# Performance work log

Measured on AMD Instinct MI355X. Metric: run time of the kernel, lower is better.

The kernel has to match this reference:

```python
import jax, jax.numpy as jnp
import numpy as np

B, N, C, H = 16, 800, 1024, 16
NC = 128  # cached KV length from the N==128 pass
HD = C // H


def setup_inputs() -> dict:
    key = jax.random.key(0)
    ks = jax.random.split(key, 9)
    s = 0.02  # init scale for weights
    return {
        "x": jax.random.normal(ks[0], (B, N, C), jnp.float32),
        "xpos": jax.random.normal(ks[1], (B, N, C), jnp.float32),
        "k_t": jax.random.normal(ks[2], (B, NC, C), jnp.float32),
        "v_t": jax.random.normal(ks[3], (B, NC, C), jnp.float32),
        "Wq": jax.random.normal(ks[4], (C, C), jnp.float32) * s,
        "Wk": jax.random.normal(ks[5], (C, C), jnp.float32) * s,
        "Wv": jax.random.normal(ks[6], (C, C), jnp.float32) * s,
        "Wp": jax.random.normal(ks[7], (C, C), jnp.float32) * s,
        "bp": jnp.zeros((C,), jnp.float32),
    }


def reference(x, xpos, k_t, v_t, Wq, Wk, Wv, Wp, bp):
    # N == 800 branch: q from x+xpos; k/v concat cached k_t/v_t before projection.
    b, n, c = x.shape
    scale = HD ** -0.5

    q = (x + xpos) @ Wq.T                              # [B, N, C]
    k_in = jnp.concatenate([x + xpos, k_t], axis=1)    # [B, N+NC, C]
    v_in = jnp.concatenate([x, v_t], axis=1)           # [B, N+NC, C]
    k = k_in @ Wk.T
    v = v_in @ Wv.T

    def heads(t):
        return t.reshape(b, t.shape[1], H, HD).transpose(0, 2, 1, 3)  # [B,H,L,HD]

    qh, kh, vh = heads(q), heads(k), heads(v)
    attn = jax.nn.softmax(jnp.einsum('bhqd,bhkd->bhqk', qh, kh) * scale, axis=-1)
    out = jnp.einsum('bhqk,bhkd->bhqd', attn, vh)       # [B,H,N,HD]
    out = out.transpose(0, 2, 1, 3).reshape(b, n, c)
    return out @ Wp.T + bp
```

## Files before the change

kernel.cpp:

```cpp
#include <hip/hip_runtime.h>
#include <hip/hip_bf16.h>

#define NB 16
#define NN 800
#define NCACHE 128
#define NL 928
#define CC 1024
#define NH 16
#define HD 64

typedef __attribute__((ext_vector_type(8))) short bf16x8;
typedef __attribute__((ext_vector_type(4))) float f32x4;
typedef __attribute__((ext_vector_type(2))) __bf16 bf2;

__device__ __forceinline__ short f2bf(float x) {
  union { float f; unsigned u; } c; c.f = x;
  unsigned r = c.u + 0x7fffu + ((c.u >> 16) & 1u);
  return (short)(r >> 16);
}

#define GLD_LDS(gp, lp) __builtin_amdgcn_global_load_lds( \
    (__attribute__((address_space(1))) void*)(gp),        \
    (__attribute__((address_space(3))) void*)(lp), 16, 0, 0)

#define BAR() asm volatile("s_barrier" ::: "memory")

__global__ __launch_bounds__(256) void prep_kv(
    const float* __restrict__ x, const float* __restrict__ xpos,
    const float* __restrict__ ktc, const float* __restrict__ vtc,
    short* __restrict__ k_in, short* __restrict__ v_in) {
  int idx = blockIdx.x * 256 + threadIdx.x;
  int chunk = idx & 127;
  int row = idx >> 7;
  int b = row / NL;
  int lr = row - b * NL;
  int c = chunk * 8;
  float vk[8], vv[8];
  if (lr < NN) {
    const float4* px = (const float4*)(x + ((size_t)(b * NN + lr) * CC + c));
    const float4* pp = (const float4*)(xpos + ((size_t)(b * NN + lr) * CC + c));
    float4 x0 = px[0], x1 = px[1], p0 = pp[0], p1 = pp[1];
    vv[0]=x0.x; vv[1]=x0.y; vv[2]=x0.z; vv[3]=x0.w;
    vv[4]=x1.x; vv[5]=x1.y; vv[6]=x1.z; vv[7]=x1.w;
    vk[0]=x0.x+p0.x; vk[1]=x0.y+p0.y; vk[2]=x0.z+p0.z; vk[3]=x0.w+p0.w;
    vk[4]=x1.x+p1.x; vk[5]=x1.y+p1.y; vk[6]=x1.z+p1.z; vk[7]=x1.w+p1.w;
  } else {
    const float4* pk = (const float4*)(ktc + ((size_t)(b * NCACHE + lr - NN) * CC + c));
    const float4* pv = (const float4*)(vtc + ((size_t)(b * NCACHE + lr - NN) * CC + c));
    float4 k0 = pk[0], k1 = pk[1], v0 = pv[0], v1 = pv[1];
    vk[0]=k0.x; vk[1]=k0.y; vk[2]=k0.z; vk[3]=k0.w;
    vk[4]=k1.x; vk[5]=k1.y; vk[6]=k1.z; vk[7]=k1.w;
    vv[0]=v0.x; vv[1]=v0.y; vv[2]=v0.z; vv[3]=v0.w;
    vv[4]=v1.x; vv[5]=v1.y; vv[6]=v1.z; vv[7]=v1.w;
  }
  bf16x8 ok, ov;
#pragma unroll
  for (int i = 0; i < 8; ++i) { ok[i] = f2bf(vk[i]); ov[i] = f2bf(vv[i]); }
  *(bf16x8*)(k_in + (size_t)row * CC + c) = ok;
  *(bf16x8*)(v_in + (size_t)row * CC + c) = ov;
}

__global__ __launch_bounds__(256) void prep_w(
    const float* __restrict__ Wq, const float* __restrict__ Wk,
    const float* __restrict__ Wv, const float* __restrict__ Wp,
    short* __restrict__ wout) {
  int idx = blockIdx.x * 256 + threadIdx.x;
  int wsel = idx >> 17;
  int off = (idx & 131071) * 8;
  const float* src = wsel == 0 ? Wq : wsel == 1 ? Wk : wsel == 2 ? Wv : Wp;
  float sc = wsel == 0 ? 0.18033688011112042f : 1.0f;
  const float4* p = (const float4*)(src + off);
  float4 a = p[0], b = p[1];
  bf16x8 o;
  o[0]=f2bf(a.x*sc); o[1]=f2bf(a.y*sc); o[2]=f2bf(a.z*sc); o[3]=f2bf(a.w*sc);
  o[4]=f2bf(b.x*sc); o[5]=f2bf(b.y*sc); o[6]=f2bf(b.z*sc); o[7]=f2bf(b.w*sc);
  *(bf16x8*)(wout + (size_t)wsel * 1048576 + off) = o;
}

#define READ_A8(dst, QR) \
  _Pragma("unroll") \
  for (int fr = 0; fr < 4; ++fr) \
    _Pragma("unroll") \
    for (int ks = 0; ks < 2; ++ks) \
      dst[fr][ks] = *(const bf16x8*)&lds[abase + (QR)*4096 + fr*1024 + (ks ? xk1 : xk0)];

#define READ_B8() \
  _Pragma("unroll") \
  for (int q = 0; q < 4; ++q) \
    _Pragma("unroll") \
    for (int ks = 0; ks < 2; ++ks) \
      bfv[q][ks] = *(const bf16x8*)&lds[bbase + q*1024 + (ks ? xk1 : xk0)];

#define MFMA_HALF(QR, asrc) \
  _Pragma("unroll") \
  for (int fr = 0; fr < 4; ++fr) \
    _Pragma("unroll") \
    for (int fc = 0; fc < 4; ++fc) \
      _Pragma("unroll") \
      for (int ks = 0; ks < 2; ++ks) \
        acc[(QR)*4+fr][fc] = __builtin_amdgcn_mfma_f32_16x16x32_bf16( \
            asrc[fr][ks], bfv[fc][ks], acc[(QR)*4+fr][fc], 0, 0, 0);

template<int MODE>
__global__ __launch_bounds__(512, 2) void gemm256(
    const short* __restrict__ A, const short* __restrict__ Bw,
    short* __restrict__ o0, short* __restrict__ o1,
    float* __restrict__ of, const float* __restrict__ bias) {
  __shared__ short lds[65536];
  const int tid = threadIdx.x;
  const int w = tid >> 6, l = tid & 63;
  const int wm = w >> 2, wn = w & 3;
  const int c = l & 15, g2 = l >> 4;
  const int BNT = (MODE == 2) ? 8 : 4;
  const int cpx = gridDim.x >> 3;
  const int swz = (blockIdx.x & 7) * cpx + (blockIdx.x >> 3);
  const int bm = swz / BNT, bn = swz % BNT;
  const int m0 = bm * 256, n0 = bn * 256;

  const int R0 = tid >> 3;
  const int gc0 = (tid & 7) ^ (R0 & 7);
  const short* As_ = A + (size_t)(m0 + R0) * CC + gc0 * 8;
  const short* Bs_ = Bw + (size_t)(n0 + R0) * CC + gc0 * 8;
  const int wofs = w * 512;

#define STAGE_HT(slot, src) do { \
    GLD_LDS((src), &lds[(slot) + wofs]); \
    GLD_LDS((src) + 64 * CC, &lds[(slot) + 4096 + wofs]); } while (0)

  const int xk0 = ((g2) ^ (c & 7)) * 8;
  const int xk1 = ((g2 + 4) ^ (c & 7)) * 8;

  f32x4 acc[8][4] = {};

  STAGE_HT(0,     As_);
  STAGE_HT(8192,  As_ + 128 * CC);
  STAGE_HT(16384, Bs_);
  STAGE_HT(24576, Bs_ + 128 * CC);

#pragma unroll 1
  for (int t = 0; t < 16; ++t) {
    const int pb = (t & 1) << 15;
    const int pn = pb ^ 32768;
    if (t < 15) {
      const short* as1 = As_ + (t + 1) * 64;
      const short* bs1 = Bs_ + (t + 1) * 64;
      STAGE_HT(pn,         as1);
      STAGE_HT(pn + 8192,  as1 + 128 * CC);
      STAGE_HT(pn + 16384, bs1);
      STAGE_HT(pn + 24576, bs1 + 128 * CC);
      asm volatile("s_waitcnt vmcnt(8)" ::: "memory");
    } else {
      asm volatile("s_waitcnt vmcnt(0)" ::: "memory");
    }
    BAR();
    const int abase = pb + wm * 8192 + c * 64;
    const int bbase = pb + 16384 + ((wn >> 1) << 13) + ((wn & 1) * 64 + c) * 64;
    bf16x8 afA[4][2], afB[4][2], bfv[4][2];
    READ_A8(afA, 0);
    READ_B8();
    __builtin_amdgcn_s_setprio(1);
    MFMA_HALF(0, afA);
    __builtin_amdgcn_s_setprio(0);
    READ_A8(afB, 1);
    __builtin_amdgcn_s_setprio(1);
    MFMA_HALF(1, afB);
    __builtin_amdgcn_s_setprio(0);
    BAR();
  }

#pragma unroll
  for (int fr = 0; fr < 8; ++fr)
#pragma unroll
    for (int fc = 0; fc < 4; ++fc) {
      const int row = m0 + wm * 128 + fr * 16 + g2 * 4;
      const int colw = wn * 64 + fc * 16 + c;
      if (MODE == 1) {
        const int col = n0 + colw;
        const float bv = bias[col];
#pragma unroll
        for (int j = 0; j < 4; ++j)
          of[(size_t)(row + j) * CC + col] = acc[fr][fc][j] + bv;
      } else if (MODE == 2) {
        const int col2 = n0 + colw;
        short* base = (col2 < 1024) ? o0 : o1;
        const int col = col2 & 1023;
#pragma unroll
        for (int j = 0; j < 4; ++j)
          base[(size_t)(row + j) * CC + col] = f2bf(acc[fr][fc][j]);
      } else {
        const int col = n0 + colw;
        const int b = row / NL;
        const int rb = row - b * NL;
        const int vtrow = (b * NH + (col >> 6)) * HD + (col & 63);
        ushort4 pk4;
        pk4.x = (unsigned short)f2bf(acc[fr][fc][0]);
        pk4.y = (unsigned short)f2bf(acc[fr][fc][1]);
        pk4.z = (unsigned short)f2bf(acc[fr][fc][2]);
        pk4.w = (unsigned short)f2bf(acc[fr][fc][3]);
        *(ushort4*)(o0 + (size_t)vtrow * NL + rb) = pk4;
      }
    }
}

__global__ __launch_bounds__(256, 3) void attn_fwd(
    const short* __restrict__ qb, const short* __restrict__ kbuf,
    const short* __restrict__ vtb, short* __restrict__ ob) {
  __shared__ short smem[2][8192];
  const int tid = threadIdx.x;
  const int w = tid >> 6;
  const int l = tid & 63;
  const int c = l & 15, g = l >> 4;
  const int swzb = (blockIdx.x & 7) * 224 + (blockIdx.x >> 3);
  const int bh = swzb / 7;
  const int blk7 = swzb - bh * 7;
  const int h = bh & 15, b = bh >> 4;
  const int q0 = blk7 * 128 + w * 32;
  const bool active = q0 < NN;

  const int r = tid >> 3, ch = tid & 7;
  const int b16 = r & 15;
  const int rp = 8 * (b16 >> 2) + (b16 & 3) + 4 * (r >> 4);
  const int xch = ch ^ (r & 7);
  const int tid8 = tid * 8;
  const short* srcKA = kbuf + (size_t)(b * NL + rp) * CC + h * HD + xch * 8;
  const short* srcVA = vtb + (size_t)(bh * HD + r) * NL + xch * 8;
  const short* srcVB = vtb + (size_t)(bh * HD + 32 + r) * NL + xch * 8;

  bf16x8 qf[2][2];
  if (active) {
#pragma unroll
    for (int f = 0; f < 2; ++f) {
      const short* qrow = qb + ((size_t)(b * NL + q0 + f * 16 + c) * CC + h * HD + g * 8);
      qf[f][0] = *(const bf16x8*)qrow;
      qf[f][1] = *(const bf16x8*)(qrow + 32);
    }
  }

  int xrc[2];
#pragma unroll
  for (int ks = 0; ks < 2; ++ks)
    xrc[ks] = (((ks * 4 + g) ^ (c & 7)) << 3);

  f32x4 acc[2][4] = {};
  f32x4 ellv[2] = {};

  auto STG_FULL = [&](int buf, int t) {
    GLD_LDS(srcKA + (size_t)(t * 64) * CC,      &smem[buf][tid8]);
    GLD_LDS(srcKA + (size_t)(t * 64 + 32) * CC, &smem[buf][2048 + tid8]);
    GLD_LDS(srcVA + t * 64,                     &smem[buf][4096 + tid8]);
    GLD_LDS(srcVB + t * 64,                     &smem[buf][6144 + tid8]);
  };
  auto STG_TAIL = [&](int buf) {
    GLD_LDS(srcKA + (size_t)896 * CC, &smem[buf][tid8]);
    const int voff = (xch < 4) ? 896 : 864;
    GLD_LDS(srcVA + voff, &smem[buf][4096 + tid8]);
    GLD_LDS(srcVB + voff, &smem[buf][6144 + tid8]);
  };

  auto COMP_FULL = [&](const short* S) {
    bf16x8 kd[4][2], vf[4][2];
#pragma unroll
    for (int si = 0; si < 4; ++si)
#pragma unroll
      for (int ks = 0; ks < 2; ++ks)
        kd[si][ks] = *(const bf16x8*)&S[si * 1024 + c * 64 + xrc[ks]];
#pragma unroll
    for (int n = 0; n < 4; ++n)
#pragma unroll
      for (int ks = 0; ks < 2; ++ks)
        vf[n][ks] = *(const bf16x8*)&S[4096 + (n * 16 + c) * 64 + xrc[ks]];
    __builtin_amdgcn_s_setprio(1);
#pragma unroll
    for (int f = 0; f < 2; ++f) {
      f32x4 z = {0.f, 0.f, 0.f, 0.f};
      f32x4 s[4];
#pragma unroll
      for (int si = 0; si < 4; ++si) {
        s[si] = __builtin_amdgcn_mfma_f32_16x16x32_bf16(kd[si][0], qf[f][0], z, 0, 0, 0);
        s[si] = __builtin_amdgcn_mfma_f32_16x16x32_bf16(kd[si][1], qf[f][1], s[si], 0, 0, 0);
      }
      f32x4 e[4];
#pragma unroll
      for (int si = 0; si < 4; ++si)
#pragma unroll
        for (int j = 0; j < 4; ++j)
          e[si][j] = __builtin_amdgcn_exp2f(s[si][j]);
      ellv[f] += (e[0] + e[1]) + (e[2] + e[3]);
      union { bf2 h2[4]; bf16x8 v; } p0, p1;
      p0.h2[0] = bf2{(__bf16)e[0][0], (__bf16)e[0][1]};
      p0.h2[1] = bf2{(__bf16)e[0][2], (__bf16)e[0][3]};
      p0.h2[2] = bf2{(__bf16)e[1][0], (__bf16)e[1][1]};
      p0.h2[3] = bf2{(__bf16)e[1][2], (__bf16)e[1][3]};
      p1.h2[0] = bf2{(__bf16)e[2][0], (__bf16)e[2][1]};
      p1.h2[1] = bf2{(__bf16)e[2][2], (__bf16)e[2][3]};
      p1.h2[2] = bf2{(__bf16)e[3][0], (__bf16)e[3][1]};
      p1.h2[3] = bf2{(__bf16)e[3][2], (__bf16)e[3][3]};
#pragma unroll
      for (int n = 0; n < 4; ++n) {
        acc[f][n] = __builtin_amdgcn_mfma_f32_16x16x32_bf16(p0.v, vf[n][0], acc[f][n], 0, 0, 0);
        acc[f][n] = __builtin_amdgcn_mfma_f32_16x16x32_bf16(p1.v, vf[n][1], acc[f][n], 0, 0, 0);
      }
    }
    __builtin_amdgcn_s_setprio(0);
  };

  auto COMP_TAIL = [&](const short* S) {
    bf16x8 kd[2][2], vf[4];
#pragma unroll
    for (int si = 0; si < 2; ++si)
#pragma unroll
      for (int ks = 0; ks < 2; ++ks)
        kd[si][ks] = *(const bf16x8*)&S[si * 1024 + c * 64 + xrc[ks]];
#pragma unroll
    for (int n = 0; n < 4; ++n)
      vf[n] = *(const bf16x8*)&S[4096 + (n * 16 + c) * 64 + xrc[0]];
#pragma unroll
    for (int f = 0; f < 2; ++f) {
      f32x4 z = {0.f, 0.f, 0.f, 0.f};
      f32x4 s[2];
#pragma unroll
      for (int si = 0; si < 2; ++si) {
        s[si] = __builtin_amdgcn_mfma_f32_16x16x32_bf16(kd[si][0], qf[f][0], z, 0, 0, 0);
        s[si] = __builtin_amdgcn_mfma_f32_16x16x32_bf16(kd[si][1], qf[f][1], s[si], 0, 0, 0);
      }
      f32x4 e0, e1;
#pragma unroll
      for (int j = 0; j < 4; ++j) { e0[j] = __builtin_amdgcn_exp2f(s[0][j]);
                                    e1[j] = __builtin_amdgcn_exp2f(s[1][j]); }
      ellv[f] += e0 + e1;
      union { bf2 h2[4]; bf16x8 v; } p0;
      p0.h2[0] = bf2{(__bf16)e0[0], (__bf16)e0[1]};
      p0.h2[1] = bf2{(__bf16)e0[2], (__bf16)e0[3]};
      p0.h2[2] = bf2{(__bf16)e1[0], (__bf16)e1[1]};
      p0.h2[3] = bf2{(__bf16)e1[2], (__bf16)e1[3]};
#pragma unroll
      for (int n = 0; n < 4; ++n)
        acc[f][n] = __builtin_amdgcn_mfma_f32_16x16x32_bf16(p0.v, vf[n], acc[f][n], 0, 0, 0);
    }
  };

  STG_FULL(0, 0);
  __syncthreads();
  int buf = 0;
  for (int t = 0; t < 14; ++t) {
    if (t < 13) STG_FULL(buf ^ 1, t + 1);
    else        STG_TAIL(buf ^ 1);
    if (active) COMP_FULL(smem[buf]);
    __syncthreads();
    buf ^= 1;
  }
  if (active) {
    COMP_TAIL(smem[buf]);
    float rinv[2];
#pragma unroll
    for (int f = 0; f < 2; ++f) {
      float e = (ellv[f][0] + ellv[f][1]) + (ellv[f][2] + ellv[f][3]);
      e += __shfl_xor(e, 16);
      e += __shfl_xor(e, 32);
      rinv[f] = 1.0f / e;
    }
#pragma unroll
    for (int f = 0; f < 2; ++f) {
      float rj[4];
#pragma unroll
      for (int j = 0; j < 4; ++j) rj[j] = __shfl(rinv[f], g * 4 + j);
      short* orow = ob + (size_t)(b * NN + q0 + f * 16 + g * 4) * CC + h * HD + c;
#pragma unroll
      for (int n = 0; n < 4; ++n)
#pragma unroll
        for (int j = 0; j < 4; ++j)
          orow[(size_t)j * CC + n * 16] = f2bf(acc[f][n][j] * rj[j]);
    }
  }
}

extern "C" void kernel_launch(void* const* d_in, const int* in_sizes, int n_in,
                              void* d_out, int out_size, void* d_ws, size_t ws_size,
                              hipStream_t stream) {
  const float* x    = (const float*)d_in[0];
  const float* xpos = (const float*)d_in[1];
  const float* k_t  = (const float*)d_in[2];
  const float* v_t  = (const float*)d_in[3];
  const float* Wq   = (const float*)d_in[4];
  const float* Wk   = (const float*)d_in[5];
  const float* Wv   = (const float*)d_in[6];
  const float* Wp   = (const float*)d_in[7];
  const float* bp   = (const float*)d_in[8];
  float* out = (float*)d_out;

  char* ws = (char*)d_ws;
  short* k_in = (short*)ws;
  short* v_in = (short*)(ws + 30408704);
  short* wqb  = (short*)(ws + 60817408);
  short* wvb  = (short*)(ws + 65011712);
  short* wpb  = (short*)(ws + 67108864);
  short* qbuf = (short*)(ws + 69206016);
  short* kbuf = (short*)(ws + 99614720);
  short* vtb  = (short*)(ws + 130023424);
  short* attn_o = k_in;

  prep_kv<<<7424, 256, 0, stream>>>(x, xpos, k_t, v_t, k_in, v_in);
  prep_w<<<2048, 256, 0, stream>>>(Wq, Wk, Wv, Wp, wqb);
  gemm256<2><<<464, 512, 0, stream>>>(k_in, wqb, qbuf, kbuf, nullptr, nullptr);
  gemm256<3><<<232, 512, 0, stream>>>(v_in, wvb, vtb, nullptr, nullptr, nullptr);
  attn_fwd<<<1792, 256, 0, stream>>>(qbuf, kbuf, vtb, attn_o);
  gemm256<1><<<200, 512, 0, stream>>>(attn_o, wpb, nullptr, nullptr, out, bp);
}
```

Measured before the change: 247.0 us.

## Pre-swizzle weights into MFMA fragment order and shrink GEMM tiles to 128

The weight-prep kernel now writes the bf16 weights in the exact per-lane MFMA fragment order. The GEMM can then load B operands straight from global memory into registers and skip staging them through LDS. The GEMM tile drops from 256x256 with 512 threads to 128x128 with 256 threads, so LDS use and the grids change (4x more blocks) for better occupancy and wave coverage on the small M. The cost is that B is re-read from global/L2 by every block, and each block loses tile-level data reuse.

Measured after the change: 251.1 us. No clear change (+1.7%).

```diff
diff --git a/kernel.cpp b/kernel.cpp
--- a/kernel.cpp
+++ b/kernel.cpp
@@ -65,115 +65,124 @@
     const float* __restrict__ Wv, const float* __restrict__ Wp,
     short* __restrict__ wout) {
   int idx = blockIdx.x * 256 + threadIdx.x;
-  int wsel = idx >> 17;
-  int off = (idx & 131071) * 8;
-  const float* src = wsel == 0 ? Wq : wsel == 1 ? Wk : wsel == 2 ? Wv : Wp;
-  float sc = wsel == 0 ? 0.18033688011112042f : 1.0f;
-  const float4* p = (const float4*)(src + off);
+  int l = idx & 63;
+  int frag = idx >> 6;
+  const float* src;
+  int col, t, ks;
+  float sc = 1.0f;
+  if (frag < 4096) {
+    ks = frag & 1; int nf = (frag >> 1) & 127; t = frag >> 8;
+    col = nf * 16 + (l & 15);
+    if (col < 1024) { src = Wq; sc = 0.18033688011112042f; }
+    else            { src = Wk; col -= 1024; }
+  } else if (frag < 6144) {
+    int f2 = frag - 4096; ks = f2 & 1; int nf = (f2 >> 1) & 63; t = f2 >> 7;
+    col = nf * 16 + (l & 15); src = Wv;
+  } else {
+    int f2 = frag - 6144; ks = f2 & 1; int nf = (f2 >> 1) & 63; t = f2 >> 7;
+    col = nf * 16 + (l & 15); src = Wp;
+  }
+  int k = t * 64 + ks * 32 + ((l >> 4) << 3);
+  const float4* p = (const float4*)(src + (size_t)col * CC + k);
   float4 a = p[0], b = p[1];
   bf16x8 o;
   o[0]=f2bf(a.x*sc); o[1]=f2bf(a.y*sc); o[2]=f2bf(a.z*sc); o[3]=f2bf(a.w*sc);
   o[4]=f2bf(b.x*sc); o[5]=f2bf(b.y*sc); o[6]=f2bf(b.z*sc); o[7]=f2bf(b.w*sc);
-  *(bf16x8*)(wout + (size_t)wsel * 1048576 + off) = o;
-}
-
-#define READ_A8(dst, QR) \
+  *(bf16x8*)(wout + (size_t)idx * 8) = o;
+}
+
+#define READ_A4(dst, FR0) \
   _Pragma("unroll") \
-  for (int fr = 0; fr < 4; ++fr) \
+  for (int fr = 0; fr < 2; ++fr) \
     _Pragma("unroll") \
     for (int ks = 0; ks < 2; ++ks) \
-      dst[fr][ks] = *(const bf16x8*)&lds[abase + (QR)*4096 + fr*1024 + (ks ? xk1 : xk0)];
-
-#define READ_B8() \
+      dst[fr][ks] = *(const bf16x8*)&lds[pb + (wr*64 + ((FR0)+fr)*16 + c)*64 \
+                                         + (ks ? xk1 : xk0)];
+
+#define MFMA_HALF(FR0, asrc) \
   _Pragma("unroll") \
-  for (int q = 0; q < 4; ++q) \
-    _Pragma("unroll") \
-    for (int ks = 0; ks < 2; ++ks) \
-      bfv[q][ks] = *(const bf16x8*)&lds[bbase + q*1024 + (ks ? xk1 : xk0)];
-
-#define MFMA_HALF(QR, asrc) \
-  _Pragma("unroll") \
-  for (int fr = 0; fr < 4; ++fr) \
+  for (int fr = 0; fr < 2; ++fr) \
     _Pragma("unroll") \
     for (int fc = 0; fc < 4; ++fc) \
       _Pragma("unroll") \
       for (int ks = 0; ks < 2; ++ks) \
-        acc[(QR)*4+fr][fc] = __builtin_amdgcn_mfma_f32_16x16x32_bf16( \
-            asrc[fr][ks], bfv[fc][ks], acc[(QR)*4+fr][fc], 0, 0, 0);
+        acc[(FR0)+fr][fc] = __builtin_amdgcn_mfma_f32_16x16x32_bf16( \
+            asrc[fr][ks], bfv[fc][ks], acc[(FR0)+fr][fc], 0, 0, 0);
 
 template<int MODE>
-__global__ __launch_bounds__(512, 2) void gemm256(
+__global__ __launch_bounds__(256, 3) void gemm128(
     const short* __restrict__ A, const short* __restrict__ Bw,
     short* __restrict__ o0, short* __restrict__ o1,
     float* __restrict__ of, const float* __restrict__ bias) {
-  __shared__ short lds[65536];
+  __shared__ short lds[16384];
   const int tid = threadIdx.x;
   const int w = tid >> 6, l = tid & 63;
-  const int wm = w >> 2, wn = w & 3;
+  const int wr = w >> 1, wc = w & 1;
   const int c = l & 15, g2 = l >> 4;
-  const int BNT = (MODE == 2) ? 8 : 4;
+  const int BNT = (MODE == 2) ? 16 : 8;
+  const int NF  = (MODE == 2) ? 128 : 64;
   const int cpx = gridDim.x >> 3;
   const int swz = (blockIdx.x & 7) * cpx + (blockIdx.x >> 3);
   const int bm = swz / BNT, bn = swz % BNT;
-  const int m0 = bm * 256, n0 = bn * 256;
-
-  const int R0 = tid >> 3;
-  const int gc0 = (tid & 7) ^ (R0 & 7);
-  const short* As_ = A + (size_t)(m0 + R0) * CC + gc0 * 8;
-  const short* Bs_ = Bw + (size_t)(n0 + R0) * CC + gc0 * 8;
-  const int wofs = w * 512;
-
-#define STAGE_HT(slot, src) do { \
-    GLD_LDS((src), &lds[(slot) + wofs]); \
-    GLD_LDS((src) + 64 * CC, &lds[(slot) + 4096 + wofs]); } while (0)
+  const int m0 = bm * 128, n0 = bn * 128;
+
+  const int rbase = w * 32 + (l >> 3);
+  const int gcA = (l & 7) ^ (l >> 3);
+  const short* As_ = A + (size_t)(m0 + rbase) * CC + gcA * 8;
+
+#define STAGE_A(par, tcol) do { \
+    _Pragma("unroll") \
+    for (int i = 0; i < 4; ++i) \
+      GLD_LDS(As_ + (size_t)(i * 8) * CC + (tcol) * 64, \
+              &lds[(par) + (w * 4 + i) * 512]); } while (0)
+
+  const int nfb = (n0 >> 4) + wc * 4;
 
   const int xk0 = ((g2) ^ (c & 7)) * 8;
   const int xk1 = ((g2 + 4) ^ (c & 7)) * 8;
 
-  f32x4 acc[8][4] = {};
-
-  STAGE_HT(0,     As_);
-  STAGE_HT(8192,  As_ + 128 * CC);
-  STAGE_HT(16384, Bs_);
-  STAGE_HT(24576, Bs_ + 128 * CC);
+  f32x4 acc[4][4] = {};
+
+  STAGE_A(0, 0);
 
 #pragma unroll 1
   for (int t = 0; t < 16; ++t) {
-    const int pb = (t & 1) << 15;
-    const int pn = pb ^ 32768;
+    const int pb = (t & 1) << 13;
+    const int pn = pb ^ 8192;
+    bf16x8 bfv[4][2];
+    {
+      const short* Bpt = Bw + (((size_t)t * NF + nfb) << 10) + (l << 3);
+#pragma unroll
+      for (int fc = 0; fc < 4; ++fc)
+#pragma unroll
+        for (int ks = 0; ks < 2; ++ks)
+          bfv[fc][ks] = *(const bf16x8*)(Bpt + ((fc << 1) | ks) * 512);
+    }
     if (t < 15) {
-      const short* as1 = As_ + (t + 1) * 64;
-      const short* bs1 = Bs_ + (t + 1) * 64;
-      STAGE_HT(pn,         as1);
-      STAGE_HT(pn + 8192,  as1 + 128 * CC);
-      STAGE_HT(pn + 16384, bs1);
-      STAGE_HT(pn + 24576, bs1 + 128 * CC);
+      STAGE_A(pn, t + 1);
+      asm volatile("s_waitcnt vmcnt(12)" ::: "memory");
+    } else {
       asm volatile("s_waitcnt vmcnt(8)" ::: "memory");
-    } else {
-      asm volatile("s_waitcnt vmcnt(0)" ::: "memory");
     }
     BAR();
-    const int abase = pb + wm * 8192 + c * 64;
-    const int bbase = pb + 16384 + ((wn >> 1) << 13) + ((wn & 1) * 64 + c) * 64;
-    bf16x8 afA[4][2], afB[4][2], bfv[4][2];
-    READ_A8(afA, 0);
-    READ_B8();
+    bf16x8 afA[2][2], afB[2][2];
+    READ_A4(afA, 0);
     __builtin_amdgcn_s_setprio(1);
     MFMA_HALF(0, afA);
     __builtin_amdgcn_s_setprio(0);
-    READ_A8(afB, 1);
+    READ_A4(afB, 2);
     __builtin_amdgcn_s_setprio(1);
-    MFMA_HALF(1, afB);
+    MFMA_HALF(2, afB);
     __builtin_amdgcn_s_setprio(0);
     BAR();
   }
 
 #pragma unroll
-  for (int fr = 0; fr < 8; ++fr)
+  for (int fr = 0; fr < 4; ++fr)
 #pragma unroll
     for (int fc = 0; fc < 4; ++fc) {
-      const int row = m0 + wm * 128 + fr * 16 + g2 * 4;
-      const int colw = wn * 64 + fc * 16 + c;
+      const int row = m0 + wr * 64 + fr * 16 + g2 * 4;
+      const int colw = wc * 64 + fc * 16 + c;
       if (MODE == 1) {
         const int col = n0 + colw;
         const float bv = bias[col];
@@ -401,8 +410,8 @@
 
   prep_kv<<<7424, 256, 0, stream>>>(x, xpos, k_t, v_t, k_in, v_in);
   prep_w<<<2048, 256, 0, stream>>>(Wq, Wk, Wv, Wp, wqb);
-  gemm256<2><<<464, 512, 0, stream>>>(k_in, wqb, qbuf, kbuf, nullptr, nullptr);
-  gemm256<3><<<232, 512, 0, stream>>>(v_in, wvb, vtb, nullptr, nullptr, nullptr);
+  gemm128<2><<<1856, 256, 0, stream>>>(k_in, wqb, qbuf, kbuf, nullptr, nullptr);
+  gemm128<3><<<928, 256, 0, stream>>>(v_in, wvb, vtb, nullptr, nullptr, nullptr);
   attn_fwd<<<1792, 256, 0, stream>>>(qbuf, kbuf, vtb, attn_o);
-  gemm256<1><<<200, 512, 0, stream>>>(attn_o, wpb, nullptr, nullptr, out, bp);
-}
+  gemm128<1><<<800, 256, 0, stream>>>(attn_o, wpb, nullptr, nullptr, out, bp);
+}
```
